# Performance work log

Measured on AMD Instinct MI355X. Metric: run time of the kernel, lower is better.

Reference implementation:

```python
import jax, jax.numpy as jnp
import numpy as np

N_NODES = 15
K = 5
L_IN = 1920
C_OUT = 256
L3 = L_IN - 3 * K + 3  # 1908
EPS = 1e-5


def setup_inputs() -> dict:
    key = jax.random.key(0)
    ks = jax.random.split(key, 18)
    B, E = 128, 56
    s = 0.05
    inp = {
        'X': jax.random.normal(ks[0], (B, N_NODES, L_IN), jnp.float32),
        'edge_index': jax.random.randint(ks[1], (2, E), 0, N_NODES),
        'edge_weight': jax.random.uniform(ks[2], (E,), jnp.float32),
        # grouped conv params (groups = N_NODES): per-group channels 1->16->32->1
        'conv1_w': jax.random.normal(ks[3], (16 * N_NODES, 1, K), jnp.float32) * s,
        'conv1_b': jnp.zeros((16 * N_NODES,), jnp.float32),
        'conv2_w': jax.random.normal(ks[4], (32 * N_NODES, 16, K), jnp.float32) * s,
        'conv2_b': jnp.zeros((32 * N_NODES,), jnp.float32),
        'conv3_w': jax.random.normal(ks[5], (N_NODES, 32, K), jnp.float32) * s,
        'conv3_b': jnp.zeros((N_NODES,), jnp.float32),
        # GCNConv: lin weight [out,in] + bias
        'gcn_w': jax.random.normal(ks[6], (C_OUT, L3), jnp.float32) * s,
        'gcn_b': jnp.zeros((C_OUT,), jnp.float32),
        'lin1_w': jax.random.normal(ks[7], (C_OUT, L_IN), jnp.float32) * s,
        'lin1_b': jnp.zeros((C_OUT,), jnp.float32),
        # GraphNorm params
        'gn_w': jnp.ones((C_OUT,), jnp.float32),
        'gn_b': jnp.zeros((C_OUT,), jnp.float32),
        'gn_ms': jnp.ones((C_OUT,), jnp.float32),
        'out_w': jax.random.normal(ks[8], (16, C_OUT), jnp.float32) * s,
        'out_b': jnp.zeros((16,), jnp.float32),
    }
    return inp


def _gconv(x, w, b):
    # grouped valid conv1d, NCH layout
    y = jax.lax.conv_general_dilated(
        x, w, window_strides=(1,), padding='VALID',
        dimension_numbers=('NCH', 'OIH', 'NCH'),
        feature_group_count=N_NODES)
    return y + b[None, :, None]


def _gcn(x, edge_index, edge_weight, W, b):
    # x: [B, N, L3]; batched GCNConv with shared edge structure (no per-t loop)
    src, dst = edge_index[0], edge_index[1]
    loop = jnp.arange(N_NODES)
    src = jnp.concatenate([src, loop])
    dst = jnp.concatenate([dst, loop])
    ew = jnp.concatenate([edge_weight, jnp.ones((N_NODES,), edge_weight.dtype)])
    deg = jnp.zeros((N_NODES,), ew.dtype).at[dst].add(ew)  # in-degree on target
    dinv = jnp.where(deg > 0, jax.lax.rsqrt(deg), 0.0)
    norm = dinv[src] * ew * dinv[dst]  # [E']
    xl = jnp.einsum('bnf,of->bno', x, W)  # [B, N, C_OUT]
    msg = norm[None, :, None] * xl[:, src, :]  # [B, E', C_OUT]
    out = jnp.zeros_like(xl).at[:, dst, :].add(msg)
    return out + b


def reference(X, edge_index, edge_weight, conv1_w, conv1_b, conv2_w, conv2_b,
              conv3_w, conv3_b, gcn_w, gcn_b, lin1_w, lin1_b, gn_w, gn_b,
              gn_ms, out_w, out_b):
    h = jax.nn.leaky_relu(_gconv(X, conv1_w, conv1_b), 0.01)
    h = jax.nn.leaky_relu(_gconv(h, conv2_w, conv2_b), 0.01)
    h = jax.nn.leaky_relu(_gconv(h, conv3_w, conv3_b), 0.01)  # [B, N, L3]
    T = _gcn(h, edge_index, edge_weight, gcn_w, gcn_b)  # [B, N, C_OUT]
    # GraphNorm with batch=None -> single graph over dim 0
    mean = T.mean(axis=0, keepdims=True)
    out = T - mean * gn_ms
    var = (out * out).mean(axis=0, keepdims=True)
    T = gn_w * out / jnp.sqrt(var + EPS) + gn_b
    T = jax.nn.elu(T + jnp.einsum('bnl,ol->bno', X, lin1_w) + lin1_b)
    output = T.mean(axis=1)  # global_mean_pool over nodes -> [B, C_OUT]
    class_output = output @ out_w.T + out_b  # [B, 16]
    return (output, class_output)
```

## Files before the change

### kernel.cpp

```cpp
#include <hip/hip_runtime.h>

typedef unsigned short u16;
typedef unsigned int   u32;

typedef short shortx8   __attribute__((ext_vector_type(8)));
typedef float floatx4   __attribute__((ext_vector_type(4)));
typedef float floatx16  __attribute__((ext_vector_type(16)));
typedef u32   uintx2    __attribute__((ext_vector_type(2)));
typedef u32   uintx4    __attribute__((ext_vector_type(4)));

typedef u32     u32a     __attribute__((may_alias));
typedef uintx2  uintx2a  __attribute__((may_alias));
typedef uintx4  uintx4a  __attribute__((may_alias));
typedef shortx8 shortx8a __attribute__((may_alias));

__device__ __forceinline__ u16 f2bf(float f){
  union { float f; u32 i; } v; v.f = f;
  return (u16)((v.i + 0x7fffu + ((v.i >> 16) & 1u)) >> 16);
}
__device__ __forceinline__ u16 f2bf_fast(float f){
  union { float f; u32 i; } v; v.f = f;
  return (u16)((v.i + 0x8000u) >> 16);
}
__device__ __forceinline__ u32 pack2(float lo, float hi){
  union { float f; u32 i; } a, b; a.f = lo; b.f = hi;
  return __builtin_amdgcn_perm(b.i + 0x8000u, a.i + 0x8000u, 0x07060302u);
}
__device__ __forceinline__ u32 cvtpk2(float lo, float hi){
#if __has_builtin(__builtin_amdgcn_cvt_pk_bf16_f32)
  auto pv = __builtin_amdgcn_cvt_pk_bf16_f32(lo, hi);
  if constexpr (sizeof(pv) == 4){
    u32 out; __builtin_memcpy(&out, &pv, 4); return out;
  } else {
    return pack2(lo, hi);
  }
#else
  return pack2(lo, hi);
#endif
}
__device__ __forceinline__ float lrelu(float v){ return fmaxf(v, 0.01f*v); }

__global__ void __launch_bounds__(256, 4) fused_conv(
    const float* __restrict__ X,
    const float* __restrict__ w1, const float* __restrict__ b1,
    const float* __restrict__ w2, const float* __restrict__ b2,
    const float* __restrict__ w3, const float* __restrict__ b3,
    u16* __restrict__ h3p, u16* __restrict__ Xb,
    const float* __restrict__ lw, u16* __restrict__ lwb,
    const float* __restrict__ gw, u16* __restrict__ gwp){
  const int tid  = threadIdx.x;
  const int node = blockIdx.z;
  const int p0   = blockIdx.x * 120;
  const int b0   = blockIdx.y * 8;

  __shared__ __attribute__((aligned(16))) u16 sPair[2][4352];
  __shared__ __attribute__((aligned(16))) u16 sW2f[2560];
  __shared__ __attribute__((aligned(16))) u16 sW3f[160];
  __shared__ __attribute__((aligned(16))) u16 sXb[8*136];
  __shared__ float sW1[80], sB1[16], sB2[32];

  {
    const int bid = blockIdx.x + 16*(blockIdx.y + 16*blockIdx.z);
    int gid = bid*256 + tid;
    if (gid < 491520){
      lwb[gid] = f2bf(lw[gid]);
    } else {
      int g2 = gid - 491520;
      int row = g2 / 1920;
      int col = g2 - row*1920;
      gwp[g2] = (col < 1908) ? f2bf(gw[row*1908 + col]) : (u16)0;
    }
  }

  {
    const int bls = tid >> 5, i0 = tid & 31;
    const float* xrow = X  + (size_t)((b0 + bls)*15 + node)*1920;
    u16*        xbrow = Xb + (size_t)((b0 + bls)*15 + node)*1920;
    #pragma unroll
    for (int u = 0; u < 5; ++u){
      int i = i0 + 32*u;
      if (i < 136){
        int g = p0 + i;
        float xv = (g < 1920) ? xrow[g] : 0.f;
        u16 xb = f2bf_fast(xv);
        sXb[bls*136 + i] = xb;
        if (i < 120) xbrow[g] = xb;
      }
    }
    #pragma unroll
    for (int u = 0; u < 10; ++u){
      int d = tid + 256*u;
      int j = d & 7, oc = (d >> 3) & 31, kh = (d >> 8) & 1, tap = d >> 9;
      sW2f[d] = f2bf(w2[node*2560 + (oc*16 + kh*8 + j)*5 + tap]);
    }
    if (tid < 160){
      int icc = tid / 5, tp = tid - 5*icc;
      sW3f[tp*32 + icc] = f2bf(w3[node*160 + tid]);
    }
    if (tid < 80) sW1[tid] = w1[node*80 + tid];
    if (tid < 16) sB1[tid] = b1[node*16 + tid];
    if (tid < 32) sB2[tid] = b2[node*32 + tid];
    {
      const int pr = tid >> 7, idx = tid & 127;
      sPair[pr][1632 + (64 + (idx >> 5))*40 + (idx & 31)] = 0;
    }
  }
  __syncthreads();

  const int w = tid >> 6, lane = tid & 63;
  const int pw = w >> 1, ph = w & 1;
  const int m = lane & 15, quad = lane >> 4;
  const int t32 = lane & 31, kh = lane >> 5;

  shortx8 a2t[5];
  #pragma unroll
  for (int tap = 0; tap < 5; ++tap)
    a2t[tap] = *(const shortx8a*)&sW2f[((tap*2 + kh)*32 + t32)*8];

  float biasr[16];
  #pragma unroll
  for (int r = 0; r < 16; ++r)
    biasr[r] = sB2[(r&3) + 8*(r>>2) + 4*kh];

  shortx8 a3[5];
  {
    const shortx8 zv = {0,0,0,0,0,0,0,0};
    #pragma unroll
    for (int tp = 0; tp < 5; ++tp){
      shortx8 t = *(const shortx8a*)&sW3f[tp*32 + quad*8];
      a3[tp] = (m == 0) ? t : zv;
    }
  }
  const float b3v = b3[node];

  shortx8 a1h = {0,0,0,0,0,0,0,0}, a1l = {0,0,0,0,0,0,0,0};
  if (quad == 0){
    const float* wrow = sW1 + m*5;
    #pragma unroll
    for (int j = 0; j < 5; ++j){
      float wv = wrow[j];
      u16 h = f2bf(wv);
      union { u32 i; float f; } hf; hf.i = ((u32)h) << 16;
      u16 l = f2bf(wv - hf.f);
      a1h[j] = (short)h; a1l[j] = (short)l;
    }
  }
  float biasA[4];
  #pragma unroll
  for (int r = 0; r < 4; ++r) biasA[r] = sB1[quad*4 + r];

  u16* h1w = sPair[pw];
  u16* h2w = sPair[pw] + 1632;

  for (int bb = 0; bb < 4; ++bb){
    const int bl = pw + bb*2;
    const int rg = (b0 + bl)*15 + node;

    {
      const int s = tid & 127;
      if (s < 68){
        const u32* xb32 = (const u32*)sXb + bl*68;
        u32 r0 = xb32[s];
        u32 r1 = (s+1 < 68) ? xb32[s+1] : 0u;
        u32 r2 = (s+2 < 68) ? xb32[s+2] : 0u;
        u32 r3 = (s+3 < 68) ? xb32[s+3] : 0u;
        u32 r4 = (s+4 < 68) ? xb32[s+4] : 0u;
        const int te = 2*s, to = 2*s + 1;
        const int offE = (s < 34) ? te*24 + 16 : 1632 + (te - 68)*40 + 32;
        const int offO = (s < 34) ? to*24 + 16 : 1632 + (to - 68)*40 + 32;
        uintx4 ve = {r0, r1, r2, r3};
        uintx4 vo = {__builtin_amdgcn_alignbit(r1, r0, 16),
                     __builtin_amdgcn_alignbit(r2, r1, 16),
                     __builtin_amdgcn_alignbit(r3, r2, 16),
                     __builtin_amdgcn_alignbit(r4, r3, 16)};
        *(uintx4a*)(h1w + offE) = ve;
        *(uintx4a*)(h1w + offO) = vo;
      }
    }
    __syncthreads();

    #pragma unroll
    for (int tt = 0; tt < 2; ++tt){
      const int p = p0 + tt*60;

      #pragma unroll
      for (int ti = 0; ti < 3; ++ti){
        const int T = ph + 2*ti;
        if (T < 5){
          const int tr = T*16 + m;
          int row = tt*60 + tr;
          row = row > 135 ? 135 : row;
          shortx8 bfr = {0,0,0,0,0,0,0,0};
          if (quad == 0){
            const int off = (row < 68) ? row*24 + 16 : 1632 + (row - 68)*40 + 32;
            bfr = *(const shortx8a*)(h1w + off);
          }
          floatx4 acc = {biasA[0], biasA[1], biasA[2], biasA[3]};
          acc = __builtin_amdgcn_mfma_f32_16x16x32_bf16(a1l, bfr, acc, 0, 0, 0);
          acc = __builtin_amdgcn_mfma_f32_16x16x32_bf16(a1h, bfr, acc, 0, 0, 0);
          if (tr < 68){
            uintx2 pk = { cvtpk2(lrelu(acc[0]), lrelu(acc[1])),
                          cvtpk2(lrelu(acc[2]), lrelu(acc[3])) };
            *(uintx2a*)(h1w + tr*24 + quad*4) = pk;
          }
        }
      }
      __syncthreads();

      {
        const int t0 = ph*32;
        floatx16 acc;
        #pragma unroll
        for (int r = 0; r < 16; ++r) acc[r] = biasr[r];
        #pragma unroll
        for (int tap = 0; tap < 5; ++tap){
          shortx8 bfr = *(const shortx8a*)(h1w + (t0 + t32 + tap)*24 + kh*8);
          acc = __builtin_amdgcn_mfma_f32_32x32x16_bf16(a2t[tap], bfr, acc, 0, 0, 0);
        }
        u16* dst = h2w + (t0 + t32)*40;
        #pragma unroll
        for (int r = 0; r < 16; r += 2){
          float v0 = lrelu(acc[r]);
          float v1 = lrelu(acc[r+1]);
          const int oc0 = (r&3) + 8*(r>>2) + 4*kh;
          *(u32a*)(dst + oc0) = cvtpk2(v0, v1);
        }
      }
      __syncthreads();

      #pragma unroll
      for (int i = 0; i < 2; ++i){
        const int nt = 2*ph + i;
        floatx4 acc3 = {0.f,0.f,0.f,0.f};
        if (lane < 16) acc3[0] = b3v;
        #pragma unroll
        for (int tp = 0; tp < 5; ++tp){
          shortx8 bfr = *(const shortx8a*)(h2w + (nt*16 + m + tp)*40 + quad*8);
          acc3 = __builtin_amdgcn_mfma_f32_16x16x32_bf16(a3[tp], bfr, acc3, 0, 0, 0);
        }
        const int tl = nt*16 + lane;
        if (lane < 16 && tl < 60){
          const int t3 = p + tl;
          float v = lrelu(acc3[0]);
          h3p[(size_t)rg*1920 + t3] = (t3 < 1908) ? f2bf_fast(v) : (u16)0;
        }
      }
    }
  }
}

__global__ void __launch_bounds__(256) gemm_nt(
    const u16* __restrict__ A0, const u16* __restrict__ B0, float* __restrict__ O0,
    const u16* __restrict__ A1, const u16* __restrict__ B1, float* __restrict__ O1,
    float* __restrict__ gZ){
  const int job = blockIdx.z;
  const u16* A; const u16* Bm; float* O;
  if (job == 0){ A = A0; Bm = B0; O = O0; } else { A = A1; Bm = B1; O = O1; }
  __shared__ __attribute__((aligned(16))) u16 sA[64*88];
  __shared__ __attribute__((aligned(16))) u16 sB[64*88];
  const int tid = threadIdx.x;
  if (blockIdx.x == 0 && blockIdx.y == 0 && job == 0){
    #pragma unroll
    for (int u = 0; u < 30; ++u) gZ[tid + 256*u] = 0.f;
  }
  const int m0 = blockIdx.x*64, n0 = blockIdx.y*64;
  const int row = tid >> 2, kc = tid & 3;
  const int w = tid >> 6, lane = tid & 63;
  const int m = lane & 15, quad = lane >> 4;
  const int mo = (w & 1)*32, no = (w >> 1)*32;
  floatx4 acc[2][2];
  #pragma unroll
  for (int i = 0; i < 2; ++i)
    #pragma unroll
    for (int j = 0; j < 2; ++j)
      #pragma unroll
      for (int r = 0; r < 4; ++r) acc[i][j][r] = 0.f;

  const u16* ap = A  + (size_t)(m0 + row)*1920 + kc*8;
  const u16* bp = Bm + (size_t)(n0 + row)*1920 + kc*8;
  for (int kt = 0; kt < 30; ++kt){
    uintx4 va0 = *(const uintx4a*)ap;
    uintx4 va1 = *(const uintx4a*)(ap + 32);
    uintx4 vb0 = *(const uintx4a*)bp;
    uintx4 vb1 = *(const uintx4a*)(bp + 32);
    ap += 64; bp += 64;
    *(uintx4a*)&sA[row*88 + kc*8]      = va0;
    *(uintx4a*)&sA[row*88 + 32 + kc*8] = va1;
    *(uintx4a*)&sB[row*88 + kc*8]      = vb0;
    *(uintx4a*)&sB[row*88 + 32 + kc*8] = vb1;
    __syncthreads();
    #pragma unroll
    for (int ks = 0; ks < 64; ks += 32){
      const shortx8 af0 = *(const shortx8a*)&sA[(mo      + m)*88 + ks + quad*8];
      const shortx8 af1 = *(const shortx8a*)&sA[(mo + 16 + m)*88 + ks + quad*8];
      const shortx8 bf0 = *(const shortx8a*)&sB[(no      + m)*88 + ks + quad*8];
      const shortx8 bf1 = *(const shortx8a*)&sB[(no + 16 + m)*88 + ks + quad*8];
      acc[0][0] = __builtin_amdgcn_mfma_f32_16x16x32_bf16(af0, bf0, acc[0][0], 0, 0, 0);
      acc[0][1] = __builtin_amdgcn_mfma_f32_16x16x32_bf16(af0, bf1, acc[0][1], 0, 0, 0);
      acc[1][0] = __builtin_amdgcn_mfma_f32_16x16x32_bf16(af1, bf0, acc[1][0], 0, 0, 0);
      acc[1][1] = __builtin_amdgcn_mfma_f32_16x16x32_bf16(af1, bf1, acc[1][1], 0, 0, 0);
    }
    __syncthreads();
  }
  #pragma unroll
  for (int mi = 0; mi < 2; ++mi)
    #pragma unroll
    for (int ni = 0; ni < 2; ++ni)
      #pragma unroll
      for (int r = 0; r < 4; ++r){
        int rr = m0 + mo + mi*16 + quad*4 + r;
        int cc = n0 + no + ni*16 + m;
        O[(size_t)rr*256 + cc] = acc[mi][ni][r];
      }
}

__global__ void __launch_bounds__(256) gcn_agg(
    const float* __restrict__ xl, const int* __restrict__ ei,
    const float* __restrict__ ew, const float* __restrict__ gcn_b,
    float* __restrict__ Tpre, float* __restrict__ gS, float* __restrict__ gS2){
  const int b = blockIdx.x, tid = threadIdx.x;
  __shared__ float sxl[15*256];
  __shared__ float s_deg[15], s_dinv[15], s_norm[71];
  __shared__ int   s_cnt[15], s_start[16], s_fill[15], s_srcl[71];
  if (tid < 15){ s_deg[tid] = 0.f; s_cnt[tid] = 0; s_fill[tid] = 0; }
  #pragma unroll
  for (int n = 0; n < 15; ++n)
    sxl[n*256 + tid] = xl[(size_t)(b*15 + n)*256 + tid];
  __syncthreads();
  int se = 0, de = 0; float we = 0.f;
  if (tid < 71){
    if (tid < 56){ se = ei[tid]; de = ei[56 + tid]; we = ew[tid]; }
    else         { se = tid - 56; de = tid - 56; we = 1.0f; }
    atomicAdd(&s_deg[de], we);
    atomicAdd(&s_cnt[de], 1);
  }
  __syncthreads();
  if (tid < 15) s_dinv[tid] = s_deg[tid] > 0.f ? rsqrtf(s_deg[tid]) : 0.f;
  if (tid == 0){
    int a = 0;
    for (int n = 0; n < 15; ++n){ s_start[n] = a; a += s_cnt[n]; }
    s_start[15] = a;
  }
  __syncthreads();
  if (tid < 71){
    float nrm = s_dinv[se]*we*s_dinv[de];
    int pos = s_start[de] + atomicAdd(&s_fill[de], 1);
    s_srcl[pos] = se; s_norm[pos] = nrm;
  }
  __syncthreads();
  const float gb = gcn_b[tid];
  for (int n = 0; n < 15; ++n){
    float acc = gb;
    const int e0 = s_start[n], e1 = s_start[n+1];
    for (int idx = e0; idx < e1; ++idx)
      acc += s_norm[idx]*sxl[s_srcl[idx]*256 + tid];
    Tpre[(size_t)(b*15 + n)*256 + tid] = acc;
    atomicAdd(&gS [n*256 + tid], acc);
    atomicAdd(&gS2[n*256 + tid], acc*acc);
  }
}

__global__ void __launch_bounds__(256) finalize_k(
    const float* __restrict__ Tpre, const float* __restrict__ l1,
    const float* __restrict__ gS, const float* __restrict__ gS2,
    const float* __restrict__ gn_ms, const float* __restrict__ gn_w,
    const float* __restrict__ gn_b, const float* __restrict__ lin1_b,
    const float* __restrict__ out_w, const float* __restrict__ out_b,
    float* __restrict__ dout){
  const int b = blockIdx.x, tid = threadIdx.x;
  __shared__ float spool[256], spart[256];
  const float gnb = gn_b[tid], lb = lin1_b[tid];
  const float gms = gn_ms[tid], gwc = gn_w[tid];
  float acc = 0.f;
  #pragma unroll
  for (int n = 0; n < 15; ++n){
    const float s  = gS [n*256 + tid];
    const float s2 = gS2[n*256 + tid];
    const float mean = s*(1.f/128.f);
    const float mo   = mean*gms;
    float var = s2*(1.f/128.f) - 2.f*mo*mean + mo*mo;
    var = fmaxf(var, 0.f);
    const float scal = gwc*rsqrtf(var + 1e-5f);
    float t = (Tpre[(size_t)(b*15 + n)*256 + tid] - mo)*scal
              + gnb + l1[(size_t)(b*15 + n)*256 + tid] + lb;
    t = t > 0.f ? t : (__expf(t) - 1.f);
    acc += t;
  }
  const float pool = acc*(1.f/15.f);
  dout[b*256 + tid] = pool;
  spool[tid] = pool;
  __syncthreads();
  const int j = tid >> 4, q = tid & 15;
  float s = 0.f;
  for (int i = 0; i < 16; ++i){
    int cc = q + i*16;
    s += spool[cc]*out_w[j*256 + cc];
  }
  spart[tid] = s;
  __syncthreads();
  if (tid < 16){
    float tot = out_b[tid];
    #pragma unroll
    for (int i = 0; i < 16; ++i) tot += spart[tid*16 + i];
    dout[32768 + b*16 + tid] = tot;
  }
}

extern "C" void kernel_launch(void* const* d_in, const int* in_sizes, int n_in,
                              void* d_out, int out_size, void* d_ws, size_t ws_size,
                              hipStream_t stream){
  (void)in_sizes; (void)n_in; (void)out_size; (void)ws_size;
  const float* X    = (const float*)d_in[0];
  const int*   ei   = (const int*)d_in[1];
  const float* ew   = (const float*)d_in[2];
  const float* w1   = (const float*)d_in[3];
  const float* b1   = (const float*)d_in[4];
  const float* w2   = (const float*)d_in[5];
  const float* b2   = (const float*)d_in[6];
  const float* w3   = (const float*)d_in[7];
  const float* b3   = (const float*)d_in[8];
  const float* gw   = (const float*)d_in[9];
  const float* gb   = (const float*)d_in[10];
  const float* lw   = (const float*)d_in[11];
  const float* lb   = (const float*)d_in[12];
  const float* gnw  = (const float*)d_in[13];
  const float* gnb  = (const float*)d_in[14];
  const float* gnms = (const float*)d_in[15];
  const float* ow   = (const float*)d_in[16];
  const float* ob   = (const float*)d_in[17];

  char* ws = (char*)d_ws;
  u16*   h3p  = (u16*)(ws + 0);
  u16*   gwp  = (u16*)(ws + 7372800);
  u16*   Xb   = (u16*)(ws + 8355840);
  u16*   lwb  = (u16*)(ws + 15728640);
  float* xl   = (float*)(ws + 16711680);
  float* l1   = (float*)(ws + 18677760);
  float* gS   = (float*)(ws + 20643840);
  float* gS2  = (float*)(ws + 20659200);
  float* Tpre = (float*)(ws + 0);

  fused_conv<<<dim3(16, 16, 15), dim3(256), 0, stream>>>(X, w1, b1, w2, b2, w3, b3,
                                                         h3p, Xb, lw, lwb, gw, gwp);
  gemm_nt   <<<dim3(30, 4, 2),   dim3(256), 0, stream>>>(Xb, lwb, l1, h3p, gwp, xl, gS);
  gcn_agg   <<<dim3(128),        dim3(256), 0, stream>>>(xl, ei, ew, gb, Tpre, gS, gS2);
  finalize_k<<<dim3(128),        dim3(256), 0, stream>>>(Tpre, l1, gS, gS2,
                                                         gnms, gnw, gnb, lb, ow, ob,
                                                         (float*)d_out);
}
```

Before: 199.2 us.

## Give each wave its own LDS scratch and replace block barriers with wave fences

New measurement: 202.0 us. No clear change (+1.4%).

```diff
diff --git a/kernel.cpp b/kernel.cpp
--- a/kernel.cpp
+++ b/kernel.cpp
@@ -40,7 +40,12 @@
 }
 __device__ __forceinline__ float lrelu(float v){ return fmaxf(v, 0.01f*v); }
 
-__global__ void __launch_bounds__(256, 4) fused_conv(
+__device__ __forceinline__ void lds_fence(){
+  asm volatile("s_waitcnt lgkmcnt(0)" ::: "memory");
+  __builtin_amdgcn_sched_barrier(0);
+}
+
+__global__ void __launch_bounds__(256, 3) fused_conv(
     const float* __restrict__ X,
     const float* __restrict__ w1, const float* __restrict__ b1,
     const float* __restrict__ w2, const float* __restrict__ b2,
@@ -53,7 +58,7 @@
   const int p0   = blockIdx.x * 120;
   const int b0   = blockIdx.y * 8;
 
-  __shared__ __attribute__((aligned(16))) u16 sPair[2][4352];
+  __shared__ __attribute__((aligned(16))) u16 sWv[4][4352];
   __shared__ __attribute__((aligned(16))) u16 sW2f[2560];
   __shared__ __attribute__((aligned(16))) u16 sW3f[160];
   __shared__ __attribute__((aligned(16))) u16 sXb[8*136];
@@ -100,17 +105,17 @@
     if (tid < 80) sW1[tid] = w1[node*80 + tid];
     if (tid < 16) sB1[tid] = b1[node*16 + tid];
     if (tid < 32) sB2[tid] = b2[node*32 + tid];
-    {
-      const int pr = tid >> 7, idx = tid & 127;
-      sPair[pr][1632 + (64 + (idx >> 5))*40 + (idx & 31)] = 0;
-    }
   }
   __syncthreads();
 
   const int w = tid >> 6, lane = tid & 63;
-  const int pw = w >> 1, ph = w & 1;
   const int m = lane & 15, quad = lane >> 4;
   const int t32 = lane & 31, kh = lane >> 5;
+
+  u16* base = sWv[w];
+  u16* h2w  = base + 1632;
+
+  *(u32a*)(h2w + (64 + (lane >> 4))*40 + (lane & 15)*2) = 0;
 
   shortx8 a2t[5];
   #pragma unroll
@@ -149,72 +154,70 @@
   #pragma unroll
   for (int r = 0; r < 4; ++r) biasA[r] = sB1[quad*4 + r];
 
-  u16* h1w = sPair[pw];
-  u16* h2w = sPair[pw] + 1632;
-
-  for (int bb = 0; bb < 4; ++bb){
-    const int bl = pw + bb*2;
+  for (int bi = 0; bi < 2; ++bi){
+    const int bl = w + bi*4;
     const int rg = (b0 + bl)*15 + node;
 
     {
-      const int s = tid & 127;
-      if (s < 68){
-        const u32* xb32 = (const u32*)sXb + bl*68;
-        u32 r0 = xb32[s];
-        u32 r1 = (s+1 < 68) ? xb32[s+1] : 0u;
-        u32 r2 = (s+2 < 68) ? xb32[s+2] : 0u;
-        u32 r3 = (s+3 < 68) ? xb32[s+3] : 0u;
-        u32 r4 = (s+4 < 68) ? xb32[s+4] : 0u;
-        const int te = 2*s, to = 2*s + 1;
-        const int offE = (s < 34) ? te*24 + 16 : 1632 + (te - 68)*40 + 32;
-        const int offO = (s < 34) ? to*24 + 16 : 1632 + (to - 68)*40 + 32;
-        uintx4 ve = {r0, r1, r2, r3};
-        uintx4 vo = {__builtin_amdgcn_alignbit(r1, r0, 16),
-                     __builtin_amdgcn_alignbit(r2, r1, 16),
-                     __builtin_amdgcn_alignbit(r3, r2, 16),
-                     __builtin_amdgcn_alignbit(r4, r3, 16)};
-        *(uintx4a*)(h1w + offE) = ve;
-        *(uintx4a*)(h1w + offO) = vo;
-      }
-    }
-    __syncthreads();
+      const u32* xb32 = (const u32*)sXb + bl*68;
+      #pragma unroll
+      for (int rep = 0; rep < 2; ++rep){
+        const int s = rep ? (64 + lane) : lane;
+        if (!rep || lane < 4){
+          u32 r0 = xb32[s];
+          u32 r1 = (s+1 < 68) ? xb32[s+1] : 0u;
+          u32 r2 = (s+2 < 68) ? xb32[s+2] : 0u;
+          u32 r3 = (s+3 < 68) ? xb32[s+3] : 0u;
+          u32 r4 = (s+4 < 68) ? xb32[s+4] : 0u;
+          const int te = 2*s, to = 2*s + 1;
+          const int offE = (te < 68) ? te*24 + 16 : 1632 + (te - 68)*40 + 32;
+          const int offO = (to < 68) ? to*24 + 16 : 1632 + (to - 68)*40 + 32;
+          uintx4 ve = {r0, r1, r2, r3};
+          uintx4 vo = {__builtin_amdgcn_alignbit(r1, r0, 16),
+                       __builtin_amdgcn_alignbit(r2, r1, 16),
+                       __builtin_amdgcn_alignbit(r3, r2, 16),
+                       __builtin_amdgcn_alignbit(r4, r3, 16)};
+          *(uintx4a*)(base + offE) = ve;
+          *(uintx4a*)(base + offO) = vo;
+        }
+      }
+    }
+    lds_fence();
 
     #pragma unroll
     for (int tt = 0; tt < 2; ++tt){
       const int p = p0 + tt*60;
 
       #pragma unroll
-      for (int ti = 0; ti < 3; ++ti){
-        const int T = ph + 2*ti;
-        if (T < 5){
-          const int tr = T*16 + m;
-          int row = tt*60 + tr;
-          row = row > 135 ? 135 : row;
-          shortx8 bfr = {0,0,0,0,0,0,0,0};
-          if (quad == 0){
-            const int off = (row < 68) ? row*24 + 16 : 1632 + (row - 68)*40 + 32;
-            bfr = *(const shortx8a*)(h1w + off);
-          }
-          floatx4 acc = {biasA[0], biasA[1], biasA[2], biasA[3]};
-          acc = __builtin_amdgcn_mfma_f32_16x16x32_bf16(a1l, bfr, acc, 0, 0, 0);
-          acc = __builtin_amdgcn_mfma_f32_16x16x32_bf16(a1h, bfr, acc, 0, 0, 0);
-          if (tr < 68){
-            uintx2 pk = { cvtpk2(lrelu(acc[0]), lrelu(acc[1])),
-                          cvtpk2(lrelu(acc[2]), lrelu(acc[3])) };
-            *(uintx2a*)(h1w + tr*24 + quad*4) = pk;
-          }
-        }
-      }
-      __syncthreads();
-
-      {
-        const int t0 = ph*32;
+      for (int T = 0; T < 5; ++T){
+        const int tr = T*16 + m;
+        int row = tt*60 + tr;
+        row = row > 135 ? 135 : row;
+        shortx8 bfr = {0,0,0,0,0,0,0,0};
+        if (quad == 0){
+          const int off = (row < 68) ? row*24 + 16 : 1632 + (row - 68)*40 + 32;
+          bfr = *(const shortx8a*)(base + off);
+        }
+        floatx4 acc = {biasA[0], biasA[1], biasA[2], biasA[3]};
+        acc = __builtin_amdgcn_mfma_f32_16x16x32_bf16(a1l, bfr, acc, 0, 0, 0);
+        acc = __builtin_amdgcn_mfma_f32_16x16x32_bf16(a1h, bfr, acc, 0, 0, 0);
+        if (tr < 68){
+          uintx2 pk = { cvtpk2(lrelu(acc[0]), lrelu(acc[1])),
+                        cvtpk2(lrelu(acc[2]), lrelu(acc[3])) };
+          *(uintx2a*)(base + tr*24 + quad*4) = pk;
+        }
+      }
+      lds_fence();
+
+      #pragma unroll
+      for (int n2 = 0; n2 < 2; ++n2){
+        const int t0 = n2*32;
         floatx16 acc;
         #pragma unroll
         for (int r = 0; r < 16; ++r) acc[r] = biasr[r];
         #pragma unroll
         for (int tap = 0; tap < 5; ++tap){
-          shortx8 bfr = *(const shortx8a*)(h1w + (t0 + t32 + tap)*24 + kh*8);
+          shortx8 bfr = *(const shortx8a*)(base + (t0 + t32 + tap)*24 + kh*8);
           acc = __builtin_amdgcn_mfma_f32_32x32x16_bf16(a2t[tap], bfr, acc, 0, 0, 0);
         }
         u16* dst = h2w + (t0 + t32)*40;
@@ -226,11 +229,10 @@
           *(u32a*)(dst + oc0) = cvtpk2(v0, v1);
         }
       }
-      __syncthreads();
-
-      #pragma unroll
-      for (int i = 0; i < 2; ++i){
-        const int nt = 2*ph + i;
+      lds_fence();
+
+      #pragma unroll
+      for (int nt = 0; nt < 4; ++nt){
         floatx4 acc3 = {0.f,0.f,0.f,0.f};
         if (lane < 16) acc3[0] = b3v;
         #pragma unroll
```

## Split GEMM K dimension in two with atomic accumulation and double-buffered LDS

Applied to the files above, without the earlier changes.

Result: faster. 193.0 us, median of 3 (-3.1%).

```diff
diff --git a/kernel.cpp b/kernel.cpp
--- a/kernel.cpp
+++ b/kernel.cpp
@@ -47,7 +47,8 @@
     const float* __restrict__ w3, const float* __restrict__ b3,
     u16* __restrict__ h3p, u16* __restrict__ Xb,
     const float* __restrict__ lw, u16* __restrict__ lwb,
-    const float* __restrict__ gw, u16* __restrict__ gwp){
+    const float* __restrict__ gw, u16* __restrict__ gwp,
+    float* __restrict__ xlz, float* __restrict__ l1z){
   const int tid  = threadIdx.x;
   const int node = blockIdx.z;
   const int p0   = blockIdx.x * 120;
@@ -64,11 +65,13 @@
     int gid = bid*256 + tid;
     if (gid < 491520){
       lwb[gid] = f2bf(lw[gid]);
+      xlz[gid] = 0.f;
     } else {
       int g2 = gid - 491520;
       int row = g2 / 1920;
       int col = g2 - row*1920;
       gwp[g2] = (col < 1908) ? f2bf(gw[row*1908 + col]) : (u16)0;
+      l1z[g2] = 0.f;
     }
   }
 
@@ -253,13 +256,13 @@
     const u16* __restrict__ A0, const u16* __restrict__ B0, float* __restrict__ O0,
     const u16* __restrict__ A1, const u16* __restrict__ B1, float* __restrict__ O1,
     float* __restrict__ gZ){
-  const int job = blockIdx.z;
+  const int job = blockIdx.z >> 1, khf = blockIdx.z & 1;
   const u16* A; const u16* Bm; float* O;
   if (job == 0){ A = A0; Bm = B0; O = O0; } else { A = A1; Bm = B1; O = O1; }
-  __shared__ __attribute__((aligned(16))) u16 sA[64*88];
-  __shared__ __attribute__((aligned(16))) u16 sB[64*88];
+  __shared__ __attribute__((aligned(16))) u16 sA[2][64*88];
+  __shared__ __attribute__((aligned(16))) u16 sB[2][64*88];
   const int tid = threadIdx.x;
-  if (blockIdx.x == 0 && blockIdx.y == 0 && job == 0){
+  if (blockIdx.x == 0 && blockIdx.y == 0 && blockIdx.z == 0){
     #pragma unroll
     for (int u = 0; u < 30; ++u) gZ[tid + 256*u] = 0.f;
   }
@@ -276,31 +279,39 @@
       #pragma unroll
       for (int r = 0; r < 4; ++r) acc[i][j][r] = 0.f;
 
-  const u16* ap = A  + (size_t)(m0 + row)*1920 + kc*8;
-  const u16* bp = Bm + (size_t)(n0 + row)*1920 + kc*8;
-  for (int kt = 0; kt < 30; ++kt){
-    uintx4 va0 = *(const uintx4a*)ap;
-    uintx4 va1 = *(const uintx4a*)(ap + 32);
-    uintx4 vb0 = *(const uintx4a*)bp;
-    uintx4 vb1 = *(const uintx4a*)(bp + 32);
-    ap += 64; bp += 64;
-    *(uintx4a*)&sA[row*88 + kc*8]      = va0;
-    *(uintx4a*)&sA[row*88 + 32 + kc*8] = va1;
-    *(uintx4a*)&sB[row*88 + kc*8]      = vb0;
-    *(uintx4a*)&sB[row*88 + 32 + kc*8] = vb1;
+  const u16* ap = A  + (size_t)(m0 + row)*1920 + khf*960 + kc*8;
+  const u16* bp = Bm + (size_t)(n0 + row)*1920 + khf*960 + kc*8;
+  uintx4 va0 = *(const uintx4a*)ap;
+  uintx4 va1 = *(const uintx4a*)(ap + 32);
+  uintx4 vb0 = *(const uintx4a*)bp;
+  uintx4 vb1 = *(const uintx4a*)(bp + 32);
+  ap += 64; bp += 64;
+
+  for (int kt = 0; kt < 15; ++kt){
+    const int c = kt & 1;
+    *(uintx4a*)&sA[c][row*88 + kc*8]      = va0;
+    *(uintx4a*)&sA[c][row*88 + 32 + kc*8] = va1;
+    *(uintx4a*)&sB[c][row*88 + kc*8]      = vb0;
+    *(uintx4a*)&sB[c][row*88 + 32 + kc*8] = vb1;
     __syncthreads();
+    if (kt < 14){
+      va0 = *(const uintx4a*)ap;
+      va1 = *(const uintx4a*)(ap + 32);
+      vb0 = *(const uintx4a*)bp;
+      vb1 = *(const uintx4a*)(bp + 32);
+      ap += 64; bp += 64;
+    }
     #pragma unroll
     for (int ks = 0; ks < 64; ks += 32){
-      const shortx8 af0 = *(const shortx8a*)&sA[(mo      + m)*88 + ks + quad*8];
-      const shortx8 af1 = *(const shortx8a*)&sA[(mo + 16 + m)*88 + ks + quad*8];
-      const shortx8 bf0 = *(const shortx8a*)&sB[(no      + m)*88 + ks + quad*8];
-      const shortx8 bf1 = *(const shortx8a*)&sB[(no + 16 + m)*88 + ks + quad*8];
+      const shortx8 af0 = *(const shortx8a*)&sA[c][(mo      + m)*88 + ks + quad*8];
+      const shortx8 af1 = *(const shortx8a*)&sA[c][(mo + 16 + m)*88 + ks + quad*8];
+      const shortx8 bf0 = *(const shortx8a*)&sB[c][(no      + m)*88 + ks + quad*8];
+      const shortx8 bf1 = *(const shortx8a*)&sB[c][(no + 16 + m)*88 + ks + quad*8];
       acc[0][0] = __builtin_amdgcn_mfma_f32_16x16x32_bf16(af0, bf0, acc[0][0], 0, 0, 0);
       acc[0][1] = __builtin_amdgcn_mfma_f32_16x16x32_bf16(af0, bf1, acc[0][1], 0, 0, 0);
       acc[1][0] = __builtin_amdgcn_mfma_f32_16x16x32_bf16(af1, bf0, acc[1][0], 0, 0, 0);
       acc[1][1] = __builtin_amdgcn_mfma_f32_16x16x32_bf16(af1, bf1, acc[1][1], 0, 0, 0);
     }
-    __syncthreads();
   }
   #pragma unroll
   for (int mi = 0; mi < 2; ++mi)
@@ -310,7 +321,7 @@
       for (int r = 0; r < 4; ++r){
         int rr = m0 + mo + mi*16 + quad*4 + r;
         int cc = n0 + no + ni*16 + m;
-        O[(size_t)rr*256 + cc] = acc[mi][ni][r];
+        atomicAdd(&O[(size_t)rr*256 + cc], acc[mi][ni][r]);
       }
 }
 
@@ -441,8 +452,9 @@
   float* Tpre = (float*)(ws + 0);
 
   fused_conv<<<dim3(16, 16, 15), dim3(256), 0, stream>>>(X, w1, b1, w2, b2, w3, b3,
-                                                         h3p, Xb, lw, lwb, gw, gwp);
-  gemm_nt   <<<dim3(30, 4, 2),   dim3(256), 0, stream>>>(Xb, lwb, l1, h3p, gwp, xl, gS);
+                                                         h3p, Xb, lw, lwb, gw, gwp,
+                                                         xl, l1);
+  gemm_nt   <<<dim3(30, 4, 4),   dim3(256), 0, stream>>>(Xb, lwb, l1, h3p, gwp, xl, gS);
   gcn_agg   <<<dim3(128),        dim3(256), 0, stream>>>(xl, ei, ew, gb, Tpre, gS, gS2);
   finalize_k<<<dim3(128),        dim3(256), 0, stream>>>(Tpre, l1, gS, gS2,
                                                          gnms, gnw, gnb, lb, ow, ob,
```
